# Kernel optimization log

Measured on AMD Instinct MI355X. Metric: run time of the kernel, lower is better.

Reference implementation:

```python
import jax, jax.numpy as jnp
import numpy as np

B, NLOC, F, H = 16384, 12, 512, 256

def setup_inputs() -> dict:
    key = jax.random.key(0)
    ks = jax.random.split(key, 8)
    s = lambda n: 1.0 / np.sqrt(n)
    return {
        "global_feature": jax.random.normal(ks[0], (B, F), jnp.float32),
        "local_features": jax.random.normal(ks[1], (B, NLOC, F), jnp.float32),
        "Wq": jax.random.normal(ks[2], (F, H), jnp.float32) * s(F),
        "bq": jnp.zeros((H,), jnp.float32),
        "Wk": jax.random.normal(ks[3], (F, H), jnp.float32) * s(F),
        "bk": jnp.zeros((H,), jnp.float32),
        "Wv": jax.random.normal(ks[4], (F, H), jnp.float32) * s(F),
        "bv": jnp.zeros((H,), jnp.float32),
        "w_dr": jax.random.normal(ks[5], (NLOC,), jnp.float32) * s(NLOC),  # Linear(12,1) weight
        "b_dr": jnp.zeros((), jnp.float32),
        "Wf": jax.random.normal(ks[6], (2 * H, F), jnp.float32) * s(2 * H),
        "bf": jnp.zeros((F,), jnp.float32),
    }

def reference(global_feature, local_features, Wq, bq, Wk, bk, Wv, bv, w_dr, b_dr, Wf, bf):
    scale = 1.0 / jnp.sqrt(jnp.float32(H))
    # dimension_reduction over the 12 local tokens: Linear(12 -> 1)
    lf_mean = jnp.einsum('bkf,k->bf', local_features, w_dr) + b_dr  # [B, F]
    # --- local queries attend to the single global token ---
    gk = global_feature @ Wk + bk                       # [B, H]
    gv = global_feature @ Wv + bv                       # [B, H]
    lq = local_features @ Wq + bq                       # [B, 12, H]
    s1 = (jnp.einsum('bkh,bh->bk', lq, gk) * scale)[..., None]  # [B, 12, 1]
    a1 = jax.nn.softmax(s1, axis=-1)                    # softmax over length-1 key axis
    weighted_global = a1 * gv[:, None, :]               # [B, 12, H]
    # --- global query attends over the 12 local tokens ---
    gq = global_feature @ Wq + bq                       # [B, H]
    lk = local_features @ Wk + bk                       # [B, 12, H]
    lv = local_features @ Wv + bv                       # [B, 12, H]
    s2 = jnp.einsum('bh,bkh->bk', gq, lk) * scale       # [B, 12]
    a2 = jax.nn.softmax(s2, axis=-1)
    local_to_global = jnp.einsum('bk,bkh->bh', a2, lv)  # [B, H]
    # pool the 12-token axis of the weighted global feature
    wg_mean = jnp.einsum('bkh,k->bh', weighted_global, w_dr) + b_dr  # [B, H]
    combined = jnp.concatenate([local_to_global, wg_mean], axis=-1)  # [B, 2H]
    fused = jax.nn.relu(combined @ Wf + bf) + lf_mean + global_feature  # [B, F]
    return fused
```

## Files before the change

### kernel.cpp

```cpp
#include <hip/hip_runtime.h>

#define NLOC 12
#define F_DIM 512
#define H_DIM 256

typedef float f4 __attribute__((ext_vector_type(4)));
typedef _Float16 half4 __attribute__((ext_vector_type(4)));
typedef _Float16 half8 __attribute__((ext_vector_type(8)));

#define OFF_W1   0ul
#define OFF_W2   (OFF_W1 + 512ul*512*2)
#define OFF_C1   (OFF_W2 + 512ul*1024*2)
#define OFF_CVEC (OFF_C1 + 2048ul)
#define OFF_ACAT (OFF_CVEC + 2048ul)
#define OFF_BASE (OFF_ACAT + 16384ul*1024*2)

__global__ void __launch_bounds__(256) precompute_w(
    const float* __restrict__ Wq, const float* __restrict__ Wk,
    const float* __restrict__ Wv, const float* __restrict__ Wf,
    const float* __restrict__ wdr,
    _Float16* __restrict__ W1, _Float16* __restrict__ W2)
{
    __shared__ float X[32][264];
    __shared__ float Y[32][264];
    const int mode = blockIdx.z;
    const int f0 = blockIdx.x * 32;
    const int j0 = blockIdx.y * 32;
    const int t = threadIdx.x;

    {
        const int r = t >> 3, cb = (t & 7) * 32;
        const float* ysrc = ((mode == 0) ? Wq : Wv) + (j0 + r) * H_DIM + cb;
#pragma unroll
        for (int u = 0; u < 32; u += 4)
            *(f4*)&Y[r][cb + u] = *(const f4*)(ysrc + u);
        if (mode == 0) {
            const float* xsrc = Wk + (f0 + r) * H_DIM + cb;
#pragma unroll
            for (int u = 0; u < 32; u += 4)
                *(f4*)&X[r][cb + u] = *(const f4*)(xsrc + u);
        }
    }
    if (mode != 0) {
        const int h = t;
        const int hoff = (mode == 2) ? H_DIM : 0;
        const float* xsrc = Wf + (long)(h + hoff) * F_DIM + f0;
        f4 v[8];
#pragma unroll
        for (int u = 0; u < 8; ++u) v[u] = *(const f4*)(xsrc + u * 4);
#pragma unroll
        for (int r = 0; r < 32; ++r) X[r][h] = v[r >> 2][r & 3];
    }
    __syncthreads();

    const int fy = t >> 4, jx = t & 15;
    float a00 = 0.f, a01 = 0.f, a10 = 0.f, a11 = 0.f;
#pragma unroll 8
    for (int h = 0; h < H_DIM; ++h) {
        float x0 = X[fy][h], x1 = X[fy + 16][h];
        float y0 = Y[jx][h], y1 = Y[jx + 16][h];
        a00 += x0 * y0; a01 += x0 * y1; a10 += x1 * y0; a11 += x1 * y1;
    }
    if (mode == 2) {
        float S = 0.f;
#pragma unroll
        for (int k = 0; k < NLOC; ++k) S += wdr[k];
        a00 *= S; a01 *= S; a10 *= S; a11 *= S;
    }
    if (mode == 0) {
        W1[(f0 + fy) * F_DIM + (j0 + jx)]             = (_Float16)a00;
        W1[(f0 + fy) * F_DIM + (j0 + jx + 16)]        = (_Float16)a01;
        W1[(f0 + fy + 16) * F_DIM + (j0 + jx)]        = (_Float16)a10;
        W1[(f0 + fy + 16) * F_DIM + (j0 + jx + 16)]   = (_Float16)a11;
    } else {
        const long co = (mode == 2) ? F_DIM : 0;
        W2[(long)(f0 + fy) * 1024 + co + (j0 + jx)]           = (_Float16)a00;
        W2[(long)(f0 + fy) * 1024 + co + (j0 + jx + 16)]      = (_Float16)a01;
        W2[(long)(f0 + fy + 16) * 1024 + co + (j0 + jx)]      = (_Float16)a10;
        W2[(long)(f0 + fy + 16) * 1024 + co + (j0 + jx + 16)] = (_Float16)a11;
    }
}

__global__ void __launch_bounds__(256) cvec_kernel(
    const float* __restrict__ Wk, const float* __restrict__ Wf,
    const float* __restrict__ bq, const float* __restrict__ bv,
    const float* __restrict__ wdr, const float* __restrict__ bdr,
    const float* __restrict__ bfv,
    float* __restrict__ c1, float* __restrict__ cvec)
{
    const int f = blockIdx.x * 256 + threadIdx.x;
    f4 a = {0.f, 0.f, 0.f, 0.f};
    const f4* wk4 = (const f4*)(Wk + (long)f * H_DIM);
    const f4* bq4 = (const f4*)bq;
#pragma unroll 4
    for (int h4 = 0; h4 < H_DIM / 4; ++h4) a += wk4[h4] * bq4[h4];
    c1[f] = a[0] + a[1] + a[2] + a[3];

    float s1 = 0.f, s2 = 0.f, s3 = 0.f;
#pragma unroll 4
    for (int h = 0; h < H_DIM; ++h) {
        float w1v = Wf[h * F_DIM + f];
        float w2v = Wf[(H_DIM + h) * F_DIM + f];
        float bvh = bv[h];
        s1 += bvh * w1v; s2 += bvh * w2v; s3 += w2v;
    }
    float S = 0.f;
#pragma unroll
    for (int k = 0; k < NLOC; ++k) S += wdr[k];
    cvec[f] = s1 + S * s2 + bdr[0] * s3 + bfv[f];
}

__global__ void __launch_bounds__(256) fused_local(
    const float* __restrict__ g, const float* __restrict__ loc,
    const _Float16* __restrict__ W1, const float* __restrict__ c1,
    const float* __restrict__ wdr, const float* __restrict__ bdr,
    _Float16* __restrict__ Acat, _Float16* __restrict__ base)
{
    __shared__ _Float16 G[32][520];
    __shared__ _Float16 T[32][520];
    __shared__ _Float16 Bs[128][40];
    const int tid = threadIdx.x;
    const int lane = tid & 63;
    const int wave = tid >> 6;
    const int quad = lane >> 4;
    const int l16 = lane & 15;
    const long m0 = (long)blockIdx.x * 32;

    {
        const int r = tid >> 3;
        const int cb = (tid & 7) * 8;
#pragma unroll
        for (int u = 0; u < 512; u += 64) {
            const float* src = g + (m0 + r) * F_DIM + cb + u;
            f4 v0 = *(const f4*)(src);
            f4 v1 = *(const f4*)(src + 4);
            half8 hv;
#pragma unroll
            for (int j = 0; j < 4; ++j) { hv[j] = (_Float16)v0[j]; hv[4 + j] = (_Float16)v1[j]; }
            *(half8*)&G[r][cb + u] = hv;
        }
    }
    __syncthreads();

    const int srB = tid >> 1, scB = (tid & 1) * 16;
    const int wn1 = wave * 32;
    for (int nt = 0; nt < 4; ++nt) {
        const int n0 = nt * 128;
        f4 acc[2][2] = {{{0.f,0.f,0.f,0.f},{0.f,0.f,0.f,0.f}},
                        {{0.f,0.f,0.f,0.f},{0.f,0.f,0.f,0.f}}};
        for (int k0 = 0; k0 < 512; k0 += 32) {
            const _Float16* wsrc = W1 + (n0 + srB) * F_DIM + k0 + scB;
            uint4 w0 = *(const uint4*)(wsrc);
            uint4 w1 = *(const uint4*)(wsrc + 8);
            *(uint4*)&Bs[srB][scB] = w0;
            *(uint4*)&Bs[srB][scB + 8] = w1;
            __syncthreads();
            half8 a0 = *(const half8*)&G[l16][k0 + quad * 8];
            half8 a1 = *(const half8*)&G[16 + l16][k0 + quad * 8];
            half8 b0 = *(const half8*)&Bs[wn1 + l16][quad * 8];
            half8 b1 = *(const half8*)&Bs[wn1 + 16 + l16][quad * 8];
            acc[0][0] = __builtin_amdgcn_mfma_f32_16x16x32_f16(a0, b0, acc[0][0], 0, 0, 0);
            acc[0][1] = __builtin_amdgcn_mfma_f32_16x16x32_f16(a0, b1, acc[0][1], 0, 0, 0);
            acc[1][0] = __builtin_amdgcn_mfma_f32_16x16x32_f16(a1, b0, acc[1][0], 0, 0, 0);
            acc[1][1] = __builtin_amdgcn_mfma_f32_16x16x32_f16(a1, b1, acc[1][1], 0, 0, 0);
            __syncthreads();
        }
#pragma unroll
        for (int ni = 0; ni < 2; ++ni) {
            const int col = n0 + wn1 + ni * 16 + l16;
            const float cv = c1[col];
#pragma unroll
            for (int mi = 0; mi < 2; ++mi)
#pragma unroll
                for (int i = 0; i < 4; ++i)
                    T[mi * 16 + quad * 4 + i][col] = (_Float16)(acc[mi][ni][i] + cv);
        }
    }
    __syncthreads();

    const int c0 = lane * 4;
    const int c1i = 256 + lane * 4;
    const float bd = bdr[0];
    float wv[NLOC];
#pragma unroll
    for (int k = 0; k < NLOC; ++k) wv[k] = wdr[k];

    for (int rr = 0; rr < 8; ++rr) {
        const int bl = wave * 8 + rr;
        const long b = m0 + bl;
        const float* lb = loc + b * (NLOC * F_DIM);

        f4 la[NLOC], lbv[NLOC];
#pragma unroll
        for (int k = 0; k < NLOC; ++k) {
            la[k]  = *(const f4*)(lb + k * F_DIM + c0);
            lbv[k] = *(const f4*)(lb + k * F_DIM + c1i);
        }
        f4 taf = __builtin_convertvector(*(const half4*)&T[bl][c0], f4);
        f4 tbf = __builtin_convertvector(*(const half4*)&T[bl][c1i], f4);

        float p[NLOC];
#pragma unroll
        for (int k = 0; k < NLOC; ++k) {
            f4 prod = la[k] * taf + lbv[k] * tbf;
            p[k] = prod[0] + prod[1] + prod[2] + prod[3];
        }
#pragma unroll
        for (int k = 0; k < NLOC; ++k) {
            float v = p[k];
            v += __shfl_xor(v, 1);
            v += __shfl_xor(v, 2);
            v += __shfl_xor(v, 4);
            v += __shfl_xor(v, 8);
            v += __shfl_xor(v, 16);
            v += __shfl_xor(v, 32);
            p[k] = v * 0.0625f;
        }
        float mx = p[0];
#pragma unroll
        for (int k = 1; k < NLOC; ++k) mx = fmaxf(mx, p[k]);
        float e[NLOC], s = 0.f;
#pragma unroll
        for (int k = 0; k < NLOC; ++k) { e[k] = expf(p[k] - mx); s += e[k]; }
        const float inv = 1.f / s;

        f4 pA = {0.f,0.f,0.f,0.f}, pB = {0.f,0.f,0.f,0.f};
        f4 fA = {0.f,0.f,0.f,0.f}, fB = {0.f,0.f,0.f,0.f};
#pragma unroll
        for (int k = 0; k < NLOC; ++k) {
            const float ak = e[k] * inv;
            const float wk = wv[k];
            pA += ak * la[k]; pB += ak * lbv[k];
            fA += wk * la[k]; fB += wk * lbv[k];
        }
        half4 gA = *(const half4*)&G[bl][c0];
        half4 gB = *(const half4*)&G[bl][c1i];
        fA += bd + __builtin_convertvector(gA, f4);
        fB += bd + __builtin_convertvector(gB, f4);

        *(half4*)(Acat + b * 1024 + c0)          = __builtin_convertvector(pA, half4);
        *(half4*)(Acat + b * 1024 + c1i)         = __builtin_convertvector(pB, half4);
        *(half4*)(Acat + b * 1024 + 512 + c0)    = gA;
        *(half4*)(Acat + b * 1024 + 512 + c1i)   = gB;
        *(half4*)(base + b * F_DIM + c0)         = __builtin_convertvector(fA, half4);
        *(half4*)(base + b * F_DIM + c1i)        = __builtin_convertvector(fB, half4);
    }
}

__global__ void __launch_bounds__(256) gemm_final(
    const _Float16* __restrict__ A, const _Float16* __restrict__ Bt,
    const float* __restrict__ cvec, const _Float16* __restrict__ base,
    float* __restrict__ out)
{
    __shared__ _Float16 As[64][40];
    __shared__ _Float16 Bs[128][40];
    const int tid = threadIdx.x;
    const int lane = tid & 63;
    const int wave = tid >> 6;
    const int quad = lane >> 4;
    const int l16 = lane & 15;
    const int wm = (wave & 1) * 32;
    const int wn = (wave >> 1) * 64;
    const long m0 = (long)blockIdx.x * 64;
    const int n0 = blockIdx.y * 128;
    const int srA = tid >> 2, scA = (tid & 3) * 8;
    const int srB = tid >> 1, scB = (tid & 1) * 16;

    f4 acc[2][4];
#pragma unroll
    for (int mi = 0; mi < 2; ++mi)
#pragma unroll
        for (int nj = 0; nj < 4; ++nj) acc[mi][nj] = (f4){0.f,0.f,0.f,0.f};

    for (int k0 = 0; k0 < 1024; k0 += 32) {
        uint4 av = *(const uint4*)(A + (m0 + srA) * 1024 + k0 + scA);
        const _Float16* bsrc = Bt + (long)(n0 + srB) * 1024 + k0 + scB;
        uint4 b0v = *(const uint4*)(bsrc);
        uint4 b1v = *(const uint4*)(bsrc + 8);
        *(uint4*)&As[srA][scA] = av;
        *(uint4*)&Bs[srB][scB] = b0v;
        *(uint4*)&Bs[srB][scB + 8] = b1v;
        __syncthreads();
        half8 a0 = *(const half8*)&As[wm + l16][quad * 8];
        half8 a1 = *(const half8*)&As[wm + 16 + l16][quad * 8];
        half8 bf[4];
#pragma unroll
        for (int nj = 0; nj < 4; ++nj)
            bf[nj] = *(const half8*)&Bs[wn + nj * 16 + l16][quad * 8];
#pragma unroll
        for (int nj = 0; nj < 4; ++nj) {
            acc[0][nj] = __builtin_amdgcn_mfma_f32_16x16x32_f16(a0, bf[nj], acc[0][nj], 0, 0, 0);
            acc[1][nj] = __builtin_amdgcn_mfma_f32_16x16x32_f16(a1, bf[nj], acc[1][nj], 0, 0, 0);
        }
        __syncthreads();
    }

#pragma unroll
    for (int mi = 0; mi < 2; ++mi)
#pragma unroll
        for (int nj = 0; nj < 4; ++nj) {
            const int col = n0 + wn + nj * 16 + l16;
            const float cv = cvec[col];
#pragma unroll
            for (int i = 0; i < 4; ++i) {
                const long row = m0 + wm + mi * 16 + quad * 4 + i;
                float v = acc[mi][nj][i] + cv;
                v = fmaxf(v, 0.f) + (float)base[row * F_DIM + col];
                out[row * F_DIM + col] = v;
            }
        }
}

extern "C" void kernel_launch(void* const* d_in, const int* in_sizes, int n_in,
                              void* d_out, int out_size, void* d_ws, size_t ws_size,
                              hipStream_t stream)
{
    (void)in_sizes; (void)n_in; (void)out_size; (void)ws_size;
    const float* gf  = (const float*)d_in[0];
    const float* loc = (const float*)d_in[1];
    const float* Wq  = (const float*)d_in[2];
    const float* bq  = (const float*)d_in[3];
    const float* Wk  = (const float*)d_in[4];
    const float* Wv  = (const float*)d_in[6];
    const float* bv  = (const float*)d_in[7];
    const float* wdr = (const float*)d_in[8];
    const float* bdr = (const float*)d_in[9];
    const float* Wf  = (const float*)d_in[10];
    const float* bfv = (const float*)d_in[11];
    float* out = (float*)d_out;

    char* ws = (char*)d_ws;
    _Float16* W1   = (_Float16*)(ws + OFF_W1);
    _Float16* W2   = (_Float16*)(ws + OFF_W2);
    float*    c1   = (float*)(ws + OFF_C1);
    float*    cvec = (float*)(ws + OFF_CVEC);
    _Float16* Acat = (_Float16*)(ws + OFF_ACAT);
    _Float16* base = (_Float16*)(ws + OFF_BASE);

    precompute_w<<<dim3(16, 16, 3), 256, 0, stream>>>(Wq, Wk, Wv, Wf, wdr, W1, W2);
    cvec_kernel<<<2, 256, 0, stream>>>(Wk, Wf, bq, bv, wdr, bdr, bfv, c1, cvec);
    fused_local<<<512, 256, 0, stream>>>(gf, loc, W1, c1, wdr, bdr, Acat, base);
    gemm_final<<<dim3(256, 4), 256, 0, stream>>>(Acat, W2, cvec, base, out);
}
```

Measured before the change: 710.4 us.

## Fuse local attention and final GEMM into one kernel keeping Acat in LDS

Merges the local-attention kernel and the final projection GEMM into one kernel that processes 16 rows per block. The concatenated activation and residual base stay in shared memory instead of going through global workspace. The cvec kernel is folded into the weight precompute launch as an extra grid slice. Weight operands W1 and W2 are now read straight from global or L2 per wave without LDS staging. This removes the Acat and base round-trips and a launch, at the cost of more redundant weight traffic per block and only 16-row MFMA tiles.

```diff
diff --git a/kernel.cpp b/kernel.cpp
--- a/kernel.cpp
+++ b/kernel.cpp
@@ -12,21 +12,48 @@
 #define OFF_W2   (OFF_W1 + 512ul*512*2)
 #define OFF_C1   (OFF_W2 + 512ul*1024*2)
 #define OFF_CVEC (OFF_C1 + 2048ul)
-#define OFF_ACAT (OFF_CVEC + 2048ul)
-#define OFF_BASE (OFF_ACAT + 16384ul*1024*2)
 
 __global__ void __launch_bounds__(256) precompute_w(
     const float* __restrict__ Wq, const float* __restrict__ Wk,
     const float* __restrict__ Wv, const float* __restrict__ Wf,
-    const float* __restrict__ wdr,
-    _Float16* __restrict__ W1, _Float16* __restrict__ W2)
+    const float* __restrict__ bq, const float* __restrict__ bv,
+    const float* __restrict__ wdr, const float* __restrict__ bdr,
+    const float* __restrict__ bfv,
+    _Float16* __restrict__ W1, _Float16* __restrict__ W2,
+    float* __restrict__ c1, float* __restrict__ cvec)
 {
+    const int mode = blockIdx.z;
+    const int t = threadIdx.x;
+
+    if (mode == 3) {
+        if (blockIdx.y != 0 || blockIdx.x >= 2) return;
+        const int f = blockIdx.x * 256 + t;
+        f4 a = {0.f, 0.f, 0.f, 0.f};
+        const f4* wk4 = (const f4*)(Wk + (long)f * H_DIM);
+        const f4* bq4 = (const f4*)bq;
+#pragma unroll 4
+        for (int h4 = 0; h4 < H_DIM / 4; ++h4) a += wk4[h4] * bq4[h4];
+        c1[f] = a[0] + a[1] + a[2] + a[3];
+
+        float s1 = 0.f, s2 = 0.f, s3 = 0.f;
+#pragma unroll 4
+        for (int h = 0; h < H_DIM; ++h) {
+            float w1v = Wf[h * F_DIM + f];
+            float w2v = Wf[(H_DIM + h) * F_DIM + f];
+            float bvh = bv[h];
+            s1 += bvh * w1v; s2 += bvh * w2v; s3 += w2v;
+        }
+        float S = 0.f;
+#pragma unroll
+        for (int k = 0; k < NLOC; ++k) S += wdr[k];
+        cvec[f] = s1 + S * s2 + bdr[0] * s3 + bfv[f];
+        return;
+    }
+
     __shared__ float X[32][264];
     __shared__ float Y[32][264];
-    const int mode = blockIdx.z;
     const int f0 = blockIdx.x * 32;
     const int j0 = blockIdx.y * 32;
-    const int t = threadIdx.x;
 
     {
         const int r = t >> 3, cb = (t & 7) * 32;
@@ -81,234 +108,157 @@
     }
 }
 
-__global__ void __launch_bounds__(256) cvec_kernel(
-    const float* __restrict__ Wk, const float* __restrict__ Wf,
-    const float* __restrict__ bq, const float* __restrict__ bv,
+#define ACS 1048
+#define TS  520
+
+__global__ void __launch_bounds__(256) mega(
+    const float* __restrict__ g, const float* __restrict__ loc,
+    const _Float16* __restrict__ W1, const _Float16* __restrict__ W2,
+    const float* __restrict__ c1, const float* __restrict__ cvec,
     const float* __restrict__ wdr, const float* __restrict__ bdr,
-    const float* __restrict__ bfv,
-    float* __restrict__ c1, float* __restrict__ cvec)
+    float* __restrict__ out)
 {
-    const int f = blockIdx.x * 256 + threadIdx.x;
-    f4 a = {0.f, 0.f, 0.f, 0.f};
-    const f4* wk4 = (const f4*)(Wk + (long)f * H_DIM);
-    const f4* bq4 = (const f4*)bq;
-#pragma unroll 4
-    for (int h4 = 0; h4 < H_DIM / 4; ++h4) a += wk4[h4] * bq4[h4];
-    c1[f] = a[0] + a[1] + a[2] + a[3];
-
-    float s1 = 0.f, s2 = 0.f, s3 = 0.f;
-#pragma unroll 4
-    for (int h = 0; h < H_DIM; ++h) {
-        float w1v = Wf[h * F_DIM + f];
-        float w2v = Wf[(H_DIM + h) * F_DIM + f];
-        float bvh = bv[h];
-        s1 += bvh * w1v; s2 += bvh * w2v; s3 += w2v;
-    }
-    float S = 0.f;
-#pragma unroll
-    for (int k = 0; k < NLOC; ++k) S += wdr[k];
-    cvec[f] = s1 + S * s2 + bdr[0] * s3 + bfv[f];
-}
-
-__global__ void __launch_bounds__(256) fused_local(
-    const float* __restrict__ g, const float* __restrict__ loc,
-    const _Float16* __restrict__ W1, const float* __restrict__ c1,
-    const float* __restrict__ wdr, const float* __restrict__ bdr,
-    _Float16* __restrict__ Acat, _Float16* __restrict__ base)
-{
-    __shared__ _Float16 G[32][520];
-    __shared__ _Float16 T[32][520];
-    __shared__ _Float16 Bs[128][40];
+    __shared__ _Float16 Acat[16 * ACS];
+    __shared__ _Float16 T[16 * TS];
     const int tid = threadIdx.x;
     const int lane = tid & 63;
     const int wave = tid >> 6;
     const int quad = lane >> 4;
     const int l16 = lane & 15;
-    const long m0 = (long)blockIdx.x * 32;
-
-    {
-        const int r = tid >> 3;
-        const int cb = (tid & 7) * 8;
-#pragma unroll
-        for (int u = 0; u < 512; u += 64) {
-            const float* src = g + (m0 + r) * F_DIM + cb + u;
-            f4 v0 = *(const f4*)(src);
-            f4 v1 = *(const f4*)(src + 4);
-            half8 hv;
-#pragma unroll
-            for (int j = 0; j < 4; ++j) { hv[j] = (_Float16)v0[j]; hv[4 + j] = (_Float16)v1[j]; }
-            *(half8*)&G[r][cb + u] = hv;
-        }
-    }
-    __syncthreads();
-
-    const int srB = tid >> 1, scB = (tid & 1) * 16;
-    const int wn1 = wave * 32;
-    for (int nt = 0; nt < 4; ++nt) {
-        const int n0 = nt * 128;
-        f4 acc[2][2] = {{{0.f,0.f,0.f,0.f},{0.f,0.f,0.f,0.f}},
-                        {{0.f,0.f,0.f,0.f},{0.f,0.f,0.f,0.f}}};
+    const long m0 = (long)blockIdx.x * 16;
+
+#pragma unroll
+    for (int it = 0; it < 8; ++it) {
+        const int idx = it * 1024 + tid * 4;
+        const int row = idx >> 9;
+        const int col = idx & 511;
+        f4 v = *(const f4*)(g + (m0 + row) * F_DIM + col);
+        half4 hv;
+#pragma unroll
+        for (int j = 0; j < 4; ++j) hv[j] = (_Float16)v[j];
+        *(half4*)&Acat[row * ACS + 512 + col] = hv;
+    }
+    __syncthreads();
+
+    {
+        const int wn = wave * 128;
+        f4 acc[8];
+#pragma unroll
+        for (int nj = 0; nj < 8; ++nj) acc[nj] = (f4){0.f, 0.f, 0.f, 0.f};
         for (int k0 = 0; k0 < 512; k0 += 32) {
-            const _Float16* wsrc = W1 + (n0 + srB) * F_DIM + k0 + scB;
-            uint4 w0 = *(const uint4*)(wsrc);
-            uint4 w1 = *(const uint4*)(wsrc + 8);
-            *(uint4*)&Bs[srB][scB] = w0;
-            *(uint4*)&Bs[srB][scB + 8] = w1;
-            __syncthreads();
-            half8 a0 = *(const half8*)&G[l16][k0 + quad * 8];
-            half8 a1 = *(const half8*)&G[16 + l16][k0 + quad * 8];
-            half8 b0 = *(const half8*)&Bs[wn1 + l16][quad * 8];
-            half8 b1 = *(const half8*)&Bs[wn1 + 16 + l16][quad * 8];
-            acc[0][0] = __builtin_amdgcn_mfma_f32_16x16x32_f16(a0, b0, acc[0][0], 0, 0, 0);
-            acc[0][1] = __builtin_amdgcn_mfma_f32_16x16x32_f16(a0, b1, acc[0][1], 0, 0, 0);
-            acc[1][0] = __builtin_amdgcn_mfma_f32_16x16x32_f16(a1, b0, acc[1][0], 0, 0, 0);
-            acc[1][1] = __builtin_amdgcn_mfma_f32_16x16x32_f16(a1, b1, acc[1][1], 0, 0, 0);
-            __syncthreads();
-        }
-#pragma unroll
-        for (int ni = 0; ni < 2; ++ni) {
-            const int col = n0 + wn1 + ni * 16 + l16;
+            half8 a0 = *(const half8*)&Acat[l16 * ACS + 512 + k0 + quad * 8];
+#pragma unroll
+            for (int nj = 0; nj < 8; ++nj) {
+                half8 b = *(const half8*)(W1 + (long)(wn + nj * 16 + l16) * 512 + k0 + quad * 8);
+                acc[nj] = __builtin_amdgcn_mfma_f32_16x16x32_f16(a0, b, acc[nj], 0, 0, 0);
+            }
+        }
+#pragma unroll
+        for (int nj = 0; nj < 8; ++nj) {
+            const int col = wn + nj * 16 + l16;
             const float cv = c1[col];
 #pragma unroll
-            for (int mi = 0; mi < 2; ++mi)
-#pragma unroll
-                for (int i = 0; i < 4; ++i)
-                    T[mi * 16 + quad * 4 + i][col] = (_Float16)(acc[mi][ni][i] + cv);
-        }
-    }
-    __syncthreads();
-
-    const int c0 = lane * 4;
-    const int c1i = 256 + lane * 4;
-    const float bd = bdr[0];
-    float wv[NLOC];
-#pragma unroll
-    for (int k = 0; k < NLOC; ++k) wv[k] = wdr[k];
-
-    for (int rr = 0; rr < 8; ++rr) {
-        const int bl = wave * 8 + rr;
-        const long b = m0 + bl;
-        const float* lb = loc + b * (NLOC * F_DIM);
-
-        f4 la[NLOC], lbv[NLOC];
-#pragma unroll
-        for (int k = 0; k < NLOC; ++k) {
-            la[k]  = *(const f4*)(lb + k * F_DIM + c0);
-            lbv[k] = *(const f4*)(lb + k * F_DIM + c1i);
-        }
-        f4 taf = __builtin_convertvector(*(const half4*)&T[bl][c0], f4);
-        f4 tbf = __builtin_convertvector(*(const half4*)&T[bl][c1i], f4);
-
-        float p[NLOC];
-#pragma unroll
-        for (int k = 0; k < NLOC; ++k) {
-            f4 prod = la[k] * taf + lbv[k] * tbf;
-            p[k] = prod[0] + prod[1] + prod[2] + prod[3];
-        }
-#pragma unroll
-        for (int k = 0; k < NLOC; ++k) {
-            float v = p[k];
-            v += __shfl_xor(v, 1);
-            v += __shfl_xor(v, 2);
-            v += __shfl_xor(v, 4);
-            v += __shfl_xor(v, 8);
-            v += __shfl_xor(v, 16);
-            v += __shfl_xor(v, 32);
-            p[k] = v * 0.0625f;
-        }
-        float mx = p[0];
-#pragma unroll
-        for (int k = 1; k < NLOC; ++k) mx = fmaxf(mx, p[k]);
-        float e[NLOC], s = 0.f;
-#pragma unroll
-        for (int k = 0; k < NLOC; ++k) { e[k] = expf(p[k] - mx); s += e[k]; }
-        const float inv = 1.f / s;
-
-        f4 pA = {0.f,0.f,0.f,0.f}, pB = {0.f,0.f,0.f,0.f};
-        f4 fA = {0.f,0.f,0.f,0.f}, fB = {0.f,0.f,0.f,0.f};
-#pragma unroll
-        for (int k = 0; k < NLOC; ++k) {
-            const float ak = e[k] * inv;
-            const float wk = wv[k];
-            pA += ak * la[k]; pB += ak * lbv[k];
-            fA += wk * la[k]; fB += wk * lbv[k];
-        }
-        half4 gA = *(const half4*)&G[bl][c0];
-        half4 gB = *(const half4*)&G[bl][c1i];
-        fA += bd + __builtin_convertvector(gA, f4);
-        fB += bd + __builtin_convertvector(gB, f4);
-
-        *(half4*)(Acat + b * 1024 + c0)          = __builtin_convertvector(pA, half4);
-        *(half4*)(Acat + b * 1024 + c1i)         = __builtin_convertvector(pB, half4);
-        *(half4*)(Acat + b * 1024 + 512 + c0)    = gA;
-        *(half4*)(Acat + b * 1024 + 512 + c1i)   = gB;
-        *(half4*)(base + b * F_DIM + c0)         = __builtin_convertvector(fA, half4);
-        *(half4*)(base + b * F_DIM + c1i)        = __builtin_convertvector(fB, half4);
-    }
-}
-
-__global__ void __launch_bounds__(256) gemm_final(
-    const _Float16* __restrict__ A, const _Float16* __restrict__ Bt,
-    const float* __restrict__ cvec, const _Float16* __restrict__ base,
-    float* __restrict__ out)
-{
-    __shared__ _Float16 As[64][40];
-    __shared__ _Float16 Bs[128][40];
-    const int tid = threadIdx.x;
-    const int lane = tid & 63;
-    const int wave = tid >> 6;
-    const int quad = lane >> 4;
-    const int l16 = lane & 15;
-    const int wm = (wave & 1) * 32;
-    const int wn = (wave >> 1) * 64;
-    const long m0 = (long)blockIdx.x * 64;
-    const int n0 = blockIdx.y * 128;
-    const int srA = tid >> 2, scA = (tid & 3) * 8;
-    const int srB = tid >> 1, scB = (tid & 1) * 16;
-
-    f4 acc[2][4];
-#pragma unroll
-    for (int mi = 0; mi < 2; ++mi)
-#pragma unroll
-        for (int nj = 0; nj < 4; ++nj) acc[mi][nj] = (f4){0.f,0.f,0.f,0.f};
-
-    for (int k0 = 0; k0 < 1024; k0 += 32) {
-        uint4 av = *(const uint4*)(A + (m0 + srA) * 1024 + k0 + scA);
-        const _Float16* bsrc = Bt + (long)(n0 + srB) * 1024 + k0 + scB;
-        uint4 b0v = *(const uint4*)(bsrc);
-        uint4 b1v = *(const uint4*)(bsrc + 8);
-        *(uint4*)&As[srA][scA] = av;
-        *(uint4*)&Bs[srB][scB] = b0v;
-        *(uint4*)&Bs[srB][scB + 8] = b1v;
-        __syncthreads();
-        half8 a0 = *(const half8*)&As[wm + l16][quad * 8];
-        half8 a1 = *(const half8*)&As[wm + 16 + l16][quad * 8];
-        half8 bf[4];
-#pragma unroll
-        for (int nj = 0; nj < 4; ++nj)
-            bf[nj] = *(const half8*)&Bs[wn + nj * 16 + l16][quad * 8];
-#pragma unroll
-        for (int nj = 0; nj < 4; ++nj) {
-            acc[0][nj] = __builtin_amdgcn_mfma_f32_16x16x32_f16(a0, bf[nj], acc[0][nj], 0, 0, 0);
-            acc[1][nj] = __builtin_amdgcn_mfma_f32_16x16x32_f16(a1, bf[nj], acc[1][nj], 0, 0, 0);
-        }
-        __syncthreads();
-    }
-
-#pragma unroll
-    for (int mi = 0; mi < 2; ++mi)
-#pragma unroll
-        for (int nj = 0; nj < 4; ++nj) {
-            const int col = n0 + wn + nj * 16 + l16;
+            for (int i = 0; i < 4; ++i)
+                T[(quad * 4 + i) * TS + col] = (_Float16)(acc[nj][i] + cv);
+        }
+    }
+    __syncthreads();
+
+    {
+        const int c0 = lane * 4;
+        const int c1i = 256 + lane * 4;
+        const float bd = bdr[0];
+        float wv[NLOC];
+#pragma unroll
+        for (int k = 0; k < NLOC; ++k) wv[k] = wdr[k];
+
+#pragma unroll
+        for (int rr = 0; rr < 4; ++rr) {
+            const int bl = wave * 4 + rr;
+            const long b = m0 + bl;
+            const float* lb = loc + b * (NLOC * F_DIM);
+
+            f4 la[NLOC], lbv[NLOC];
+#pragma unroll
+            for (int k = 0; k < NLOC; ++k) {
+                la[k]  = *(const f4*)(lb + k * F_DIM + c0);
+                lbv[k] = *(const f4*)(lb + k * F_DIM + c1i);
+            }
+            f4 taf = __builtin_convertvector(*(const half4*)&T[bl * TS + c0], f4);
+            f4 tbf = __builtin_convertvector(*(const half4*)&T[bl * TS + c1i], f4);
+
+            float p[NLOC];
+#pragma unroll
+            for (int k = 0; k < NLOC; ++k) {
+                f4 prod = la[k] * taf + lbv[k] * tbf;
+                p[k] = prod[0] + prod[1] + prod[2] + prod[3];
+            }
+#pragma unroll
+            for (int k = 0; k < NLOC; ++k) {
+                float v = p[k];
+                v += __shfl_xor(v, 1);
+                v += __shfl_xor(v, 2);
+                v += __shfl_xor(v, 4);
+                v += __shfl_xor(v, 8);
+                v += __shfl_xor(v, 16);
+                v += __shfl_xor(v, 32);
+                p[k] = v * 0.0625f;
+            }
+            float mx = p[0];
+#pragma unroll
+            for (int k = 1; k < NLOC; ++k) mx = fmaxf(mx, p[k]);
+            float e[NLOC], s = 0.f;
+#pragma unroll
+            for (int k = 0; k < NLOC; ++k) { e[k] = expf(p[k] - mx); s += e[k]; }
+            const float inv = 1.f / s;
+
+            f4 pA = {0.f,0.f,0.f,0.f}, pB = {0.f,0.f,0.f,0.f};
+            f4 fA = {0.f,0.f,0.f,0.f}, fB = {0.f,0.f,0.f,0.f};
+#pragma unroll
+            for (int k = 0; k < NLOC; ++k) {
+                const float ak = e[k] * inv;
+                const float wk = wv[k];
+                pA += ak * la[k]; pB += ak * lbv[k];
+                fA += wk * la[k]; fB += wk * lbv[k];
+            }
+            f4 gA = __builtin_convertvector(*(const half4*)&Acat[bl * ACS + 512 + c0], f4);
+            f4 gB = __builtin_convertvector(*(const half4*)&Acat[bl * ACS + 512 + c1i], f4);
+            fA += bd + gA;
+            fB += bd + gB;
+
+            *(half4*)&Acat[bl * ACS + c0]  = __builtin_convertvector(pA, half4);
+            *(half4*)&Acat[bl * ACS + c1i] = __builtin_convertvector(pB, half4);
+            *(half4*)&T[bl * TS + c0]  = __builtin_convertvector(fA, half4);
+            *(half4*)&T[bl * TS + c1i] = __builtin_convertvector(fB, half4);
+        }
+    }
+    __syncthreads();
+
+    {
+        const int wn = wave * 128;
+        f4 acc[8];
+#pragma unroll
+        for (int nj = 0; nj < 8; ++nj) acc[nj] = (f4){0.f, 0.f, 0.f, 0.f};
+        for (int k0 = 0; k0 < 1024; k0 += 32) {
+            half8 a0 = *(const half8*)&Acat[l16 * ACS + k0 + quad * 8];
+#pragma unroll
+            for (int nj = 0; nj < 8; ++nj) {
+                half8 b = *(const half8*)(W2 + (long)(wn + nj * 16 + l16) * 1024 + k0 + quad * 8);
+                acc[nj] = __builtin_amdgcn_mfma_f32_16x16x32_f16(a0, b, acc[nj], 0, 0, 0);
+            }
+        }
+#pragma unroll
+        for (int nj = 0; nj < 8; ++nj) {
+            const int col = wn + nj * 16 + l16;
             const float cv = cvec[col];
 #pragma unroll
             for (int i = 0; i < 4; ++i) {
-                const long row = m0 + wm + mi * 16 + quad * 4 + i;
-                float v = acc[mi][nj][i] + cv;
-                v = fmaxf(v, 0.f) + (float)base[row * F_DIM + col];
-                out[row * F_DIM + col] = v;
-            }
-        }
+                const int rl = quad * 4 + i;
+                float v = fmaxf(acc[nj][i] + cv, 0.f) + (float)T[rl * TS + col];
+                out[(m0 + rl) * F_DIM + col] = v;
+            }
+        }
+    }
 }
 
 extern "C" void kernel_launch(void* const* d_in, const int* in_sizes, int n_in,
@@ -334,11 +284,8 @@
     _Float16* W2   = (_Float16*)(ws + OFF_W2);
     float*    c1   = (float*)(ws + OFF_C1);
     float*    cvec = (float*)(ws + OFF_CVEC);
-    _Float16* Acat = (_Float16*)(ws + OFF_ACAT);
-    _Float16* base = (_Float16*)(ws + OFF_BASE);
-
-    precompute_w<<<dim3(16, 16, 3), 256, 0, stream>>>(Wq, Wk, Wv, Wf, wdr, W1, W2);
-    cvec_kernel<<<2, 256, 0, stream>>>(Wk, Wf, bq, bv, wdr, bdr, bfv, c1, cvec);
-    fused_local<<<512, 256, 0, stream>>>(gf, loc, W1, c1, wdr, bdr, Acat, base);
-    gemm_final<<<dim3(256, 4), 256, 0, stream>>>(Acat, W2, cvec, base, out);
+
+    precompute_w<<<dim3(16, 16, 4), 256, 0, stream>>>(Wq, Wk, Wv, Wf, bq, bv,
+                                                      wdr, bdr, bfv, W1, W2, c1, cvec);
+    mega<<<1024, 256, 0, stream>>>(gf, loc, W1, W2, c1, cvec, wdr, bdr, out);
 }
```

After: 750.3 us. 5.6% more time.
